# Optimization experiments

Hardware: AMD Instinct MI355X
Metric: run time of the kernel (lower is better)

Reference implementation:

```python
import jax, jax.numpy as jnp
import numpy as np

M, N, B, S = 512, 1024, 64, 50   # measurements, signal dim, batch, sparsity
TAU, ETA = 1.0, 0.1


def setup_inputs() -> dict:
    key = jax.random.key(0)
    k1, k2, k3 = jax.random.split(key, 3)
    X = jax.random.normal(k1, (N, B), dtype=jnp.float32)
    Y = jax.random.normal(k2, (B, M), dtype=jnp.float32)
    A = jax.random.normal(k3, (M, N), dtype=jnp.float32) / np.sqrt(M).astype(np.float32)
    W = jnp.ones((N,), dtype=jnp.float32)
    return {"X": X, "Y": Y, "A": A, "W": W}


def reference(X, Y, A, W):
    # Gradient step: H1 = (I - eta A^T A) X + eta A^T Y^T, computed without
    # materializing the N x N operator.  H1: (N, B)
    H1 = X - ETA * (A.T @ (A @ X)) + ETA * (A.T @ Y.T)
    # NeuralSort soft top-s mask per sample, batched over B.
    z = jnp.abs(W[:, None] * H1).T                      # (B, N) scores
    c = jnp.sum(jnp.abs(z[:, :, None] - z[:, None, :]), axis=-1)  # (B, N)
    ks = (N + 1 - 2 * jnp.arange(1, S + 1)).astype(z.dtype)       # (S,)
    logits = (ks[None, :, None] * z[:, None, :] - c[:, None, :]) / TAU  # (B, S, N)
    mask = jnp.sum(jax.nn.softmax(logits, axis=-1), axis=1)            # (B, N)
    return mask.T * H1                                  # (N, B)
```

## Files before the change

kernel.cpp:

```cpp
#include <hip/hip_runtime.h>
#include <math.h>

#define MM 512
#define NN 1024
#define BB 64
#define SS 50
#define ETA 0.1f

__global__ __launch_bounds__(512) void k_r(const float* __restrict__ X,
                                           const float* __restrict__ Y,
                                           const float* __restrict__ A,
                                           float* __restrict__ R) {
  const int l = threadIdx.x;
  const int w = threadIdx.y;
  const int m0 = blockIdx.x * 2;
  __shared__ float part[8][2][BB];
  const float* __restrict__ Xp = X + w * 128 * BB + l;
  const float* __restrict__ A0 = A + (size_t)m0 * NN + w * 128;
  const float* __restrict__ A1 = A0 + NN;
  float r0a = 0.f, r0b = 0.f, r1a = 0.f, r1b = 0.f;
  #pragma unroll 8
  for (int i = 0; i < 128; i += 4) {
    const float x0 = Xp[(i + 0) * BB];
    const float x1 = Xp[(i + 1) * BB];
    const float x2 = Xp[(i + 2) * BB];
    const float x3 = Xp[(i + 3) * BB];
    const float4 a0 = *reinterpret_cast<const float4*>(A0 + i);
    const float4 a1 = *reinterpret_cast<const float4*>(A1 + i);
    r0a = fmaf(a0.x, x0, fmaf(a0.y, x1, r0a));
    r0b = fmaf(a0.z, x2, fmaf(a0.w, x3, r0b));
    r1a = fmaf(a1.x, x0, fmaf(a1.y, x1, r1a));
    r1b = fmaf(a1.z, x2, fmaf(a1.w, x3, r1b));
  }
  part[w][0][l] = r0a + r0b;
  part[w][1][l] = r1a + r1b;
  __syncthreads();
  if (w < 2) {
    const float s =
        ((part[0][w][l] + part[1][w][l]) + (part[2][w][l] + part[3][w][l])) +
        ((part[4][w][l] + part[5][w][l]) + (part[6][w][l] + part[7][w][l]));
    R[(m0 + w) * BB + l] = Y[l * MM + (m0 + w)] - s;
  }
}

__global__ __launch_bounds__(512) void k_h1z(const float* __restrict__ X,
                                             const float* __restrict__ A,
                                             const float* __restrict__ R,
                                             const float* __restrict__ W,
                                             float* __restrict__ H1_t,
                                             float* __restrict__ z_t) {
  const int l = threadIdx.x;
  const int w = threadIdx.y;
  const int b_l = w >> 2;
  const int mc = w & 3;
  const int nc = blockIdx.x & 7;
  const int bp = blockIdx.x >> 3;
  const int b = bp * 2 + b_l;
  const int n0 = nc * 128;
  __shared__ float part[2][4][128];
  const float* __restrict__ Ap = A + (size_t)(mc * 128) * NN + n0 + l * 2;
  const float* __restrict__ Rp = R + (size_t)(mc * 128) * BB + b;
  float s0 = 0.f, s1 = 0.f, s2 = 0.f, s3 = 0.f;
  float t0 = 0.f, t1 = 0.f, t2 = 0.f, t3 = 0.f;
  #pragma unroll 2
  for (int i = 0; i < 128; i += 4) {
    const float2 a0 = *reinterpret_cast<const float2*>(Ap + (size_t)(i + 0) * NN);
    const float2 a1 = *reinterpret_cast<const float2*>(Ap + (size_t)(i + 1) * NN);
    const float2 a2 = *reinterpret_cast<const float2*>(Ap + (size_t)(i + 2) * NN);
    const float2 a3 = *reinterpret_cast<const float2*>(Ap + (size_t)(i + 3) * NN);
    const float r0 = Rp[(i + 0) * BB];
    const float r1 = Rp[(i + 1) * BB];
    const float r2 = Rp[(i + 2) * BB];
    const float r3 = Rp[(i + 3) * BB];
    s0 = fmaf(a0.x, r0, s0); t0 = fmaf(a0.y, r0, t0);
    s1 = fmaf(a1.x, r1, s1); t1 = fmaf(a1.y, r1, t1);
    s2 = fmaf(a2.x, r2, s2); t2 = fmaf(a2.y, r2, t2);
    s3 = fmaf(a3.x, r3, s3); t3 = fmaf(a3.y, r3, t3);
  }
  part[b_l][mc][l * 2 + 0] = (s0 + s1) + (s2 + s3);
  part[b_l][mc][l * 2 + 1] = (t0 + t1) + (t2 + t3);
  __syncthreads();
  const int tid = w * 64 + l;
  if (tid < 256) {
    const int bl2 = tid >> 7;
    const int nn = tid & 127;
    const int bb = bp * 2 + bl2;
    const int n = n0 + nn;
    const float s = (part[bl2][0][nn] + part[bl2][1][nn]) +
                    (part[bl2][2][nn] + part[bl2][3][nn]);
    const float h = fmaf(ETA, s, X[n * BB + bb]);
    H1_t[bb * NN + n] = h;
    z_t[bb * NN + n] = fabsf(W[n] * h);
  }
}

__global__ __launch_bounds__(256) void k_c(const float* __restrict__ z_t,
                                           float* __restrict__ c_part) {
  const int b = blockIdx.x >> 3;
  const int q = blockIdx.x & 7;
  const int t = threadIdx.x;
  __shared__ __align__(16) float4 z4[NN / 4];
  z4[t] = reinterpret_cast<const float4*>(z_t + b * NN)[t];
  __syncthreads();
  const float* zs = reinterpret_cast<const float*>(z4);
  const float zn0 = zs[t];
  const float zn1 = zs[t + 256];
  const float zn2 = zs[t + 512];
  const float zn3 = zs[t + 768];
  float c0 = 0.f, c1 = 0.f, c2 = 0.f, c3 = 0.f;
  const float4* zq = z4 + q * 32;
  #pragma unroll 4
  for (int i = 0; i < 32; ++i) {
    const float4 f = zq[i];
    c0 += (fabsf(zn0 - f.x) + fabsf(zn0 - f.y)) + (fabsf(zn0 - f.z) + fabsf(zn0 - f.w));
    c1 += (fabsf(zn1 - f.x) + fabsf(zn1 - f.y)) + (fabsf(zn1 - f.z) + fabsf(zn1 - f.w));
    c2 += (fabsf(zn2 - f.x) + fabsf(zn2 - f.y)) + (fabsf(zn2 - f.z) + fabsf(zn2 - f.w));
    c3 += (fabsf(zn3 - f.x) + fabsf(zn3 - f.y)) + (fabsf(zn3 - f.z) + fabsf(zn3 - f.w));
  }
  float* cp = c_part + q * (BB * NN) + b * NN;
  cp[t] = c0;
  cp[t + 256] = c1;
  cp[t + 512] = c2;
  cp[t + 768] = c3;
}

__global__ __launch_bounds__(1024) void k_sm(const float* __restrict__ z_t,
                                             const float* __restrict__ c_part,
                                             const float* __restrict__ H1_t,
                                             float* __restrict__ out) {
  const int b = blockIdx.x;
  const int t = threadIdx.x;
  __shared__ __align__(16) float2 zc_s[NN];
  __shared__ float mpart[16][NN];

  const float z = z_t[b * NN + t];
  const int ci = b * NN + t;
  const int BN = BB * NN;
  const float c = ((c_part[ci] + c_part[ci + BN]) +
                   (c_part[ci + 2 * BN] + c_part[ci + 3 * BN])) +
                  ((c_part[ci + 4 * BN] + c_part[ci + 5 * BN]) +
                   (c_part[ci + 6 * BN] + c_part[ci + 7 * BN]));
  zc_s[t] = make_float2(z, c);
  const float h = H1_t[b * NN + t];
  __syncthreads();

  const int w = t >> 6;
  const int lane = t & 63;
  float zz[16], cc[16], mp[16];
  #pragma unroll
  for (int k = 0; k < 16; ++k) {
    const float2 v = zc_s[lane + 64 * k];
    zz[k] = v.x;
    cc[k] = v.y;
    mp[k] = 0.f;
  }

  for (int s = w; s < SS; s += 16) {
    const float ks = (float)(NN + 1 - 2 * (s + 1));
    float lg[16];
    float mx = -INFINITY;
    #pragma unroll
    for (int k = 0; k < 16; ++k) {
      lg[k] = fmaf(ks, zz[k], -cc[k]);
      mx = fmaxf(mx, lg[k]);
    }
    #pragma unroll
    for (int off = 32; off > 0; off >>= 1)
      mx = fmaxf(mx, __shfl_xor(mx, off, 64));
    float sum = 0.f;
    #pragma unroll
    for (int k = 0; k < 16; ++k) {
      lg[k] = __expf(lg[k] - mx);
      sum += lg[k];
    }
    #pragma unroll
    for (int off = 32; off > 0; off >>= 1)
      sum += __shfl_xor(sum, off, 64);
    const float rs = 1.f / sum;
    #pragma unroll
    for (int k = 0; k < 16; ++k) mp[k] = fmaf(lg[k], rs, mp[k]);
  }
  #pragma unroll
  for (int k = 0; k < 16; ++k) mpart[w][lane + 64 * k] = mp[k];
  __syncthreads();

  float mask = 0.f;
  #pragma unroll
  for (int u = 0; u < 16; ++u) mask += mpart[u][t];
  out[t * BB + b] = mask * h;
}

extern "C" void kernel_launch(void* const* d_in, const int* in_sizes, int n_in,
                              void* d_out, int out_size, void* d_ws, size_t ws_size,
                              hipStream_t stream) {
  const float* X = (const float*)d_in[0];
  const float* Y = (const float*)d_in[1];
  const float* A = (const float*)d_in[2];
  const float* W = (const float*)d_in[3];
  float* out = (float*)d_out;

  float* R = (float*)d_ws;
  float* z_t = R + MM * BB;
  float* H1_t = z_t + NN * BB;
  float* c_part = H1_t + NN * BB;

  k_r   <<<dim3(MM / 2), dim3(64, 8), 0, stream>>>(X, Y, A, R);
  k_h1z <<<dim3(256), dim3(64, 8), 0, stream>>>(X, A, R, W, H1_t, z_t);
  k_c   <<<dim3(BB * 8), dim3(256), 0, stream>>>(z_t, c_part);
  k_sm  <<<dim3(BB), dim3(1024), 0, stream>>>(z_t, c_part, H1_t, out);
}
```

Measured before the change: 37.13 us.

## Fuse four stage kernels into one cooperative kernel with grid syncs

Replaces the four separate launches (residual, H1/z, pairwise c, softmax mask) with a single cooperative kernel of 256 blocks of 512 threads, separated by grid.sync barriers. The goal is to remove launch gaps and inter-kernel drain between the dependent stages. In exchange, stage 3 and stage 4 are remapped to fewer, narrower blocks (4 partial c sums instead of 8, 8 waves per sample instead of 16), which lowers parallelism in those stages. Grid-wide barriers also add their own cost.

```diff
diff --git a/kernel.cpp b/kernel.cpp
--- a/kernel.cpp
+++ b/kernel.cpp
@@ -1,5 +1,8 @@
 #include <hip/hip_runtime.h>
+#include <hip/hip_cooperative_groups.h>
 #include <math.h>
+
+namespace cg = cooperative_groups;
 
 #define MM 512
 #define NN 1024
@@ -7,187 +10,185 @@
 #define SS 50
 #define ETA 0.1f
 
-__global__ __launch_bounds__(512) void k_r(const float* __restrict__ X,
-                                           const float* __restrict__ Y,
-                                           const float* __restrict__ A,
-                                           float* __restrict__ R) {
-  const int l = threadIdx.x;
-  const int w = threadIdx.y;
-  const int m0 = blockIdx.x * 2;
-  __shared__ float part[8][2][BB];
-  const float* __restrict__ Xp = X + w * 128 * BB + l;
-  const float* __restrict__ A0 = A + (size_t)m0 * NN + w * 128;
-  const float* __restrict__ A1 = A0 + NN;
-  float r0a = 0.f, r0b = 0.f, r1a = 0.f, r1b = 0.f;
-  #pragma unroll 8
-  for (int i = 0; i < 128; i += 4) {
-    const float x0 = Xp[(i + 0) * BB];
-    const float x1 = Xp[(i + 1) * BB];
-    const float x2 = Xp[(i + 2) * BB];
-    const float x3 = Xp[(i + 3) * BB];
-    const float4 a0 = *reinterpret_cast<const float4*>(A0 + i);
-    const float4 a1 = *reinterpret_cast<const float4*>(A1 + i);
-    r0a = fmaf(a0.x, x0, fmaf(a0.y, x1, r0a));
-    r0b = fmaf(a0.z, x2, fmaf(a0.w, x3, r0b));
-    r1a = fmaf(a1.x, x0, fmaf(a1.y, x1, r1a));
-    r1b = fmaf(a1.z, x2, fmaf(a1.w, x3, r1b));
-  }
-  part[w][0][l] = r0a + r0b;
-  part[w][1][l] = r1a + r1b;
-  __syncthreads();
-  if (w < 2) {
-    const float s =
-        ((part[0][w][l] + part[1][w][l]) + (part[2][w][l] + part[3][w][l])) +
-        ((part[4][w][l] + part[5][w][l]) + (part[6][w][l] + part[7][w][l]));
-    R[(m0 + w) * BB + l] = Y[l * MM + (m0 + w)] - s;
-  }
-}
-
-__global__ __launch_bounds__(512) void k_h1z(const float* __restrict__ X,
-                                             const float* __restrict__ A,
-                                             const float* __restrict__ R,
-                                             const float* __restrict__ W,
-                                             float* __restrict__ H1_t,
-                                             float* __restrict__ z_t) {
-  const int l = threadIdx.x;
-  const int w = threadIdx.y;
-  const int b_l = w >> 2;
-  const int mc = w & 3;
-  const int nc = blockIdx.x & 7;
-  const int bp = blockIdx.x >> 3;
-  const int b = bp * 2 + b_l;
-  const int n0 = nc * 128;
-  __shared__ float part[2][4][128];
-  const float* __restrict__ Ap = A + (size_t)(mc * 128) * NN + n0 + l * 2;
-  const float* __restrict__ Rp = R + (size_t)(mc * 128) * BB + b;
-  float s0 = 0.f, s1 = 0.f, s2 = 0.f, s3 = 0.f;
-  float t0 = 0.f, t1 = 0.f, t2 = 0.f, t3 = 0.f;
-  #pragma unroll 2
-  for (int i = 0; i < 128; i += 4) {
-    const float2 a0 = *reinterpret_cast<const float2*>(Ap + (size_t)(i + 0) * NN);
-    const float2 a1 = *reinterpret_cast<const float2*>(Ap + (size_t)(i + 1) * NN);
-    const float2 a2 = *reinterpret_cast<const float2*>(Ap + (size_t)(i + 2) * NN);
-    const float2 a3 = *reinterpret_cast<const float2*>(Ap + (size_t)(i + 3) * NN);
-    const float r0 = Rp[(i + 0) * BB];
-    const float r1 = Rp[(i + 1) * BB];
-    const float r2 = Rp[(i + 2) * BB];
-    const float r3 = Rp[(i + 3) * BB];
-    s0 = fmaf(a0.x, r0, s0); t0 = fmaf(a0.y, r0, t0);
-    s1 = fmaf(a1.x, r1, s1); t1 = fmaf(a1.y, r1, t1);
-    s2 = fmaf(a2.x, r2, s2); t2 = fmaf(a2.y, r2, t2);
-    s3 = fmaf(a3.x, r3, s3); t3 = fmaf(a3.y, r3, t3);
-  }
-  part[b_l][mc][l * 2 + 0] = (s0 + s1) + (s2 + s3);
-  part[b_l][mc][l * 2 + 1] = (t0 + t1) + (t2 + t3);
-  __syncthreads();
-  const int tid = w * 64 + l;
-  if (tid < 256) {
-    const int bl2 = tid >> 7;
-    const int nn = tid & 127;
-    const int bb = bp * 2 + bl2;
-    const int n = n0 + nn;
-    const float s = (part[bl2][0][nn] + part[bl2][1][nn]) +
-                    (part[bl2][2][nn] + part[bl2][3][nn]);
-    const float h = fmaf(ETA, s, X[n * BB + bb]);
-    H1_t[bb * NN + n] = h;
-    z_t[bb * NN + n] = fabsf(W[n] * h);
-  }
-}
-
-__global__ __launch_bounds__(256) void k_c(const float* __restrict__ z_t,
-                                           float* __restrict__ c_part) {
-  const int b = blockIdx.x >> 3;
-  const int q = blockIdx.x & 7;
+__global__ __launch_bounds__(512, 2) void k_fused(
+    const float* __restrict__ X,
+    const float* __restrict__ Y,
+    const float* __restrict__ A,
+    const float* __restrict__ W,
+    float* __restrict__ R,
+    float* __restrict__ z_t,
+    float* __restrict__ H1_t,
+    float* __restrict__ c_part,
+    float* __restrict__ out) {
+  cg::grid_group grid = cg::this_grid();
+  const int bid = blockIdx.x;
   const int t = threadIdx.x;
+  const int l = t & 63;
+  const int w = t >> 6;
+
+  __shared__ float p1[8][2][BB];
+  __shared__ float p2[2][4][128];
   __shared__ __align__(16) float4 z4[NN / 4];
-  z4[t] = reinterpret_cast<const float4*>(z_t + b * NN)[t];
-  __syncthreads();
-  const float* zs = reinterpret_cast<const float*>(z4);
-  const float zn0 = zs[t];
-  const float zn1 = zs[t + 256];
-  const float zn2 = zs[t + 512];
-  const float zn3 = zs[t + 768];
-  float c0 = 0.f, c1 = 0.f, c2 = 0.f, c3 = 0.f;
-  const float4* zq = z4 + q * 32;
-  #pragma unroll 4
-  for (int i = 0; i < 32; ++i) {
-    const float4 f = zq[i];
-    c0 += (fabsf(zn0 - f.x) + fabsf(zn0 - f.y)) + (fabsf(zn0 - f.z) + fabsf(zn0 - f.w));
-    c1 += (fabsf(zn1 - f.x) + fabsf(zn1 - f.y)) + (fabsf(zn1 - f.z) + fabsf(zn1 - f.w));
-    c2 += (fabsf(zn2 - f.x) + fabsf(zn2 - f.y)) + (fabsf(zn2 - f.z) + fabsf(zn2 - f.w));
-    c3 += (fabsf(zn3 - f.x) + fabsf(zn3 - f.y)) + (fabsf(zn3 - f.z) + fabsf(zn3 - f.w));
-  }
-  float* cp = c_part + q * (BB * NN) + b * NN;
-  cp[t] = c0;
-  cp[t + 256] = c1;
-  cp[t + 512] = c2;
-  cp[t + 768] = c3;
-}
-
-__global__ __launch_bounds__(1024) void k_sm(const float* __restrict__ z_t,
-                                             const float* __restrict__ c_part,
-                                             const float* __restrict__ H1_t,
-                                             float* __restrict__ out) {
-  const int b = blockIdx.x;
-  const int t = threadIdx.x;
   __shared__ __align__(16) float2 zc_s[NN];
-  __shared__ float mpart[16][NN];
-
-  const float z = z_t[b * NN + t];
-  const int ci = b * NN + t;
-  const int BN = BB * NN;
-  const float c = ((c_part[ci] + c_part[ci + BN]) +
-                   (c_part[ci + 2 * BN] + c_part[ci + 3 * BN])) +
-                  ((c_part[ci + 4 * BN] + c_part[ci + 5 * BN]) +
-                   (c_part[ci + 6 * BN] + c_part[ci + 7 * BN]));
-  zc_s[t] = make_float2(z, c);
-  const float h = H1_t[b * NN + t];
-  __syncthreads();
-
-  const int w = t >> 6;
-  const int lane = t & 63;
-  float zz[16], cc[16], mp[16];
-  #pragma unroll
-  for (int k = 0; k < 16; ++k) {
-    const float2 v = zc_s[lane + 64 * k];
-    zz[k] = v.x;
-    cc[k] = v.y;
-    mp[k] = 0.f;
-  }
-
-  for (int s = w; s < SS; s += 16) {
-    const float ks = (float)(NN + 1 - 2 * (s + 1));
-    float lg[16];
-    float mx = -INFINITY;
+  __shared__ float mpart[8][NN];
+
+  {
+    const int m0 = bid * 2;
+    const float* __restrict__ Xp = X + w * 128 * BB + l;
+    const float* __restrict__ A0 = A + (size_t)m0 * NN + w * 128;
+    const float* __restrict__ A1 = A0 + NN;
+    float r0a = 0.f, r0b = 0.f, r1a = 0.f, r1b = 0.f;
+    #pragma unroll 8
+    for (int i = 0; i < 128; i += 4) {
+      const float x0 = Xp[(i + 0) * BB];
+      const float x1 = Xp[(i + 1) * BB];
+      const float x2 = Xp[(i + 2) * BB];
+      const float x3 = Xp[(i + 3) * BB];
+      const float4 a0 = *reinterpret_cast<const float4*>(A0 + i);
+      const float4 a1 = *reinterpret_cast<const float4*>(A1 + i);
+      r0a = fmaf(a0.x, x0, fmaf(a0.y, x1, r0a));
+      r0b = fmaf(a0.z, x2, fmaf(a0.w, x3, r0b));
+      r1a = fmaf(a1.x, x0, fmaf(a1.y, x1, r1a));
+      r1b = fmaf(a1.z, x2, fmaf(a1.w, x3, r1b));
+    }
+    p1[w][0][l] = r0a + r0b;
+    p1[w][1][l] = r1a + r1b;
+    __syncthreads();
+    if (w < 2) {
+      const float s =
+          ((p1[0][w][l] + p1[1][w][l]) + (p1[2][w][l] + p1[3][w][l])) +
+          ((p1[4][w][l] + p1[5][w][l]) + (p1[6][w][l] + p1[7][w][l]));
+      R[(m0 + w) * BB + l] = Y[l * MM + (m0 + w)] - s;
+    }
+  }
+  grid.sync();
+
+  {
+    const int b_l = w >> 2;
+    const int mc = w & 3;
+    const int nc = bid & 7;
+    const int bp = bid >> 3;
+    const int b = bp * 2 + b_l;
+    const int n0 = nc * 128;
+    const float* __restrict__ Ap = A + (size_t)(mc * 128) * NN + n0 + l * 2;
+    const float* __restrict__ Rp = R + (size_t)(mc * 128) * BB + b;
+    float s0 = 0.f, s1 = 0.f, s2 = 0.f, s3 = 0.f;
+    float t0 = 0.f, t1 = 0.f, t2 = 0.f, t3 = 0.f;
+    #pragma unroll 2
+    for (int i = 0; i < 128; i += 4) {
+      const float2 a0 = *reinterpret_cast<const float2*>(Ap + (size_t)(i + 0) * NN);
+      const float2 a1 = *reinterpret_cast<const float2*>(Ap + (size_t)(i + 1) * NN);
+      const float2 a2 = *reinterpret_cast<const float2*>(Ap + (size_t)(i + 2) * NN);
+      const float2 a3 = *reinterpret_cast<const float2*>(Ap + (size_t)(i + 3) * NN);
+      const float r0 = Rp[(i + 0) * BB];
+      const float r1 = Rp[(i + 1) * BB];
+      const float r2 = Rp[(i + 2) * BB];
+      const float r3 = Rp[(i + 3) * BB];
+      s0 = fmaf(a0.x, r0, s0); t0 = fmaf(a0.y, r0, t0);
+      s1 = fmaf(a1.x, r1, s1); t1 = fmaf(a1.y, r1, t1);
+      s2 = fmaf(a2.x, r2, s2); t2 = fmaf(a2.y, r2, t2);
+      s3 = fmaf(a3.x, r3, s3); t3 = fmaf(a3.y, r3, t3);
+    }
+    p2[b_l][mc][l * 2 + 0] = (s0 + s1) + (s2 + s3);
+    p2[b_l][mc][l * 2 + 1] = (t0 + t1) + (t2 + t3);
+    __syncthreads();
+    if (t < 256) {
+      const int bl2 = t >> 7;
+      const int nn = t & 127;
+      const int bb = bp * 2 + bl2;
+      const int n = n0 + nn;
+      const float s = (p2[bl2][0][nn] + p2[bl2][1][nn]) +
+                      (p2[bl2][2][nn] + p2[bl2][3][nn]);
+      const float h = fmaf(ETA, s, X[n * BB + bb]);
+      H1_t[bb * NN + n] = h;
+      z_t[bb * NN + n] = fabsf(W[n] * h);
+    }
+  }
+  grid.sync();
+
+  {
+    const int b = bid >> 2;
+    const int q = bid & 3;
+    if (t < 256) z4[t] = reinterpret_cast<const float4*>(z_t + b * NN)[t];
+    __syncthreads();
+    const float* zs = reinterpret_cast<const float*>(z4);
+    const float zn0 = zs[t];
+    const float zn1 = zs[t + 512];
+    float c0 = 0.f, c1 = 0.f;
+    const float4* zq = z4 + q * 64;
+    #pragma unroll 4
+    for (int i = 0; i < 64; ++i) {
+      const float4 f = zq[i];
+      c0 += (fabsf(zn0 - f.x) + fabsf(zn0 - f.y)) + (fabsf(zn0 - f.z) + fabsf(zn0 - f.w));
+      c1 += (fabsf(zn1 - f.x) + fabsf(zn1 - f.y)) + (fabsf(zn1 - f.z) + fabsf(zn1 - f.w));
+    }
+    float* cp = c_part + q * (BB * NN) + b * NN;
+    cp[t] = c0;
+    cp[t + 512] = c1;
+  }
+  grid.sync();
+
+  if (bid < BB) {
+    const int b = bid;
+    const int BN = BB * NN;
+    {
+      const int i0 = b * NN + t;
+      const int i1 = i0 + 512;
+      const float cA = (c_part[i0] + c_part[i0 + BN]) +
+                       (c_part[i0 + 2 * BN] + c_part[i0 + 3 * BN]);
+      const float cB = (c_part[i1] + c_part[i1 + BN]) +
+                       (c_part[i1 + 2 * BN] + c_part[i1 + 3 * BN]);
+      zc_s[t] = make_float2(z_t[i0], cA);
+      zc_s[t + 512] = make_float2(z_t[i1], cB);
+    }
+    __syncthreads();
+
+    float zz[16], cc[16], mp[16];
     #pragma unroll
     for (int k = 0; k < 16; ++k) {
-      lg[k] = fmaf(ks, zz[k], -cc[k]);
-      mx = fmaxf(mx, lg[k]);
+      const float2 v = zc_s[l + 64 * k];
+      zz[k] = v.x;
+      cc[k] = v.y;
+      mp[k] = 0.f;
+    }
+    for (int s = w; s < SS; s += 8) {
+      const float ks = (float)(NN + 1 - 2 * (s + 1));
+      float lg[16];
+      float mx = -INFINITY;
+      #pragma unroll
+      for (int k = 0; k < 16; ++k) {
+        lg[k] = fmaf(ks, zz[k], -cc[k]);
+        mx = fmaxf(mx, lg[k]);
+      }
+      #pragma unroll
+      for (int off = 32; off > 0; off >>= 1)
+        mx = fmaxf(mx, __shfl_xor(mx, off, 64));
+      float sum = 0.f;
+      #pragma unroll
+      for (int k = 0; k < 16; ++k) {
+        lg[k] = __expf(lg[k] - mx);
+        sum += lg[k];
+      }
+      #pragma unroll
+      for (int off = 32; off > 0; off >>= 1)
+        sum += __shfl_xor(sum, off, 64);
+      const float rs = 1.f / sum;
+      #pragma unroll
+      for (int k = 0; k < 16; ++k) mp[k] = fmaf(lg[k], rs, mp[k]);
     }
     #pragma unroll
-    for (int off = 32; off > 0; off >>= 1)
-      mx = fmaxf(mx, __shfl_xor(mx, off, 64));
-    float sum = 0.f;
+    for (int k = 0; k < 16; ++k) mpart[w][l + 64 * k] = mp[k];
+    __syncthreads();
+
+    float m0 = 0.f, m1 = 0.f;
     #pragma unroll
-    for (int k = 0; k < 16; ++k) {
-      lg[k] = __expf(lg[k] - mx);
-      sum += lg[k];
-    }
-    #pragma unroll
-    for (int off = 32; off > 0; off >>= 1)
-      sum += __shfl_xor(sum, off, 64);
-    const float rs = 1.f / sum;
-    #pragma unroll
-    for (int k = 0; k < 16; ++k) mp[k] = fmaf(lg[k], rs, mp[k]);
-  }
-  #pragma unroll
-  for (int k = 0; k < 16; ++k) mpart[w][lane + 64 * k] = mp[k];
-  __syncthreads();
-
-  float mask = 0.f;
-  #pragma unroll
-  for (int u = 0; u < 16; ++u) mask += mpart[u][t];
-  out[t * BB + b] = mask * h;
+    for (int u = 0; u < 8; ++u) {
+      m0 += mpart[u][t];
+      m1 += mpart[u][t + 512];
+    }
+    out[t * BB + b] = m0 * H1_t[b * NN + t];
+    out[(t + 512) * BB + b] = m1 * H1_t[b * NN + t + 512];
+  }
 }
 
 extern "C" void kernel_launch(void* const* d_in, const int* in_sizes, int n_in,
@@ -204,8 +205,9 @@
   float* H1_t = z_t + NN * BB;
   float* c_part = H1_t + NN * BB;
 
-  k_r   <<<dim3(MM / 2), dim3(64, 8), 0, stream>>>(X, Y, A, R);
-  k_h1z <<<dim3(256), dim3(64, 8), 0, stream>>>(X, A, R, W, H1_t, z_t);
-  k_c   <<<dim3(BB * 8), dim3(256), 0, stream>>>(z_t, c_part);
-  k_sm  <<<dim3(BB), dim3(1024), 0, stream>>>(z_t, c_part, H1_t, out);
+  void* args[] = {(void*)&X, (void*)&Y, (void*)&A, (void*)&W,
+                  (void*)&R, (void*)&z_t, (void*)&H1_t, (void*)&c_part,
+                  (void*)&out};
+  hipLaunchCooperativeKernel((void*)k_fused, dim3(256), dim3(512), args, 0,
+                             stream);
 }
```

Measured after the change: 131.2 us. 3.53x slower.

## Transpose residual layout, stage it in LDS, and halve pairwise-distance split

Applied to the files above, without the earlier changes.

k_r now writes the residual transposed (batch-major) with float2 stores and float2 loads of Y. k_h1z stages two residual rows in shared memory and reads them as float4, replacing strided scalar global loads with broadcast LDS reads. k_c splits each sample into 4 chunks instead of 8, so each block does more work, k_sm sums 4 partials instead of 8, and the c_part layout becomes contiguous per sample. The trade-off is fewer blocks in k_c (256) and an extra sync in k_h1z.

```diff
diff --git a/kernel.cpp b/kernel.cpp
--- a/kernel.cpp
+++ b/kernel.cpp
@@ -10,7 +10,7 @@
 __global__ __launch_bounds__(512) void k_r(const float* __restrict__ X,
                                            const float* __restrict__ Y,
                                            const float* __restrict__ A,
-                                           float* __restrict__ R) {
+                                           float* __restrict__ R_t) {
   const int l = threadIdx.x;
   const int w = threadIdx.y;
   const int m0 = blockIdx.x * 2;
@@ -35,59 +35,72 @@
   part[w][0][l] = r0a + r0b;
   part[w][1][l] = r1a + r1b;
   __syncthreads();
-  if (w < 2) {
-    const float s =
-        ((part[0][w][l] + part[1][w][l]) + (part[2][w][l] + part[3][w][l])) +
-        ((part[4][w][l] + part[5][w][l]) + (part[6][w][l] + part[7][w][l]));
-    R[(m0 + w) * BB + l] = Y[l * MM + (m0 + w)] - s;
+  if (w == 0) {
+    const float s0 =
+        ((part[0][0][l] + part[1][0][l]) + (part[2][0][l] + part[3][0][l])) +
+        ((part[4][0][l] + part[5][0][l]) + (part[6][0][l] + part[7][0][l]));
+    const float s1 =
+        ((part[0][1][l] + part[1][1][l]) + (part[2][1][l] + part[3][1][l])) +
+        ((part[4][1][l] + part[5][1][l]) + (part[6][1][l] + part[7][1][l]));
+    const float2 y2 = *reinterpret_cast<const float2*>(Y + l * MM + m0);
+    *reinterpret_cast<float2*>(R_t + l * MM + m0) =
+        make_float2(y2.x - s0, y2.y - s1);
   }
 }
 
 __global__ __launch_bounds__(512) void k_h1z(const float* __restrict__ X,
                                              const float* __restrict__ A,
-                                             const float* __restrict__ R,
+                                             const float* __restrict__ R_t,
                                              const float* __restrict__ W,
                                              float* __restrict__ H1_t,
                                              float* __restrict__ z_t) {
   const int l = threadIdx.x;
   const int w = threadIdx.y;
+  const int nc = blockIdx.x & 7;
+  const int bp = blockIdx.x >> 3;
+  const int t5 = w * 64 + l;
+  __shared__ __align__(16) float Rs[2][MM];
+  __shared__ float p2[2][4][128];
+
+  if (t5 < 256) {
+    const int row = t5 >> 7;
+    const int idx = t5 & 127;
+    reinterpret_cast<float4*>(Rs[row])[idx] =
+        reinterpret_cast<const float4*>(R_t + (size_t)(bp * 2 + row) * MM)[idx];
+  }
+  __syncthreads();
+
   const int b_l = w >> 2;
   const int mc = w & 3;
-  const int nc = blockIdx.x & 7;
-  const int bp = blockIdx.x >> 3;
-  const int b = bp * 2 + b_l;
   const int n0 = nc * 128;
-  __shared__ float part[2][4][128];
-  const float* __restrict__ Ap = A + (size_t)(mc * 128) * NN + n0 + l * 2;
-  const float* __restrict__ Rp = R + (size_t)(mc * 128) * BB + b;
+  const float2* __restrict__ A2 =
+      reinterpret_cast<const float2*>(A) + (size_t)(mc * 128) * (NN / 2) + n0 / 2 + l;
+  const float4* __restrict__ R4 =
+      reinterpret_cast<const float4*>(Rs[b_l]) + mc * 32;
   float s0 = 0.f, s1 = 0.f, s2 = 0.f, s3 = 0.f;
-  float t0 = 0.f, t1 = 0.f, t2 = 0.f, t3 = 0.f;
+  float u0 = 0.f, u1 = 0.f, u2 = 0.f, u3 = 0.f;
   #pragma unroll 2
   for (int i = 0; i < 128; i += 4) {
-    const float2 a0 = *reinterpret_cast<const float2*>(Ap + (size_t)(i + 0) * NN);
-    const float2 a1 = *reinterpret_cast<const float2*>(Ap + (size_t)(i + 1) * NN);
-    const float2 a2 = *reinterpret_cast<const float2*>(Ap + (size_t)(i + 2) * NN);
-    const float2 a3 = *reinterpret_cast<const float2*>(Ap + (size_t)(i + 3) * NN);
-    const float r0 = Rp[(i + 0) * BB];
-    const float r1 = Rp[(i + 1) * BB];
-    const float r2 = Rp[(i + 2) * BB];
-    const float r3 = Rp[(i + 3) * BB];
-    s0 = fmaf(a0.x, r0, s0); t0 = fmaf(a0.y, r0, t0);
-    s1 = fmaf(a1.x, r1, s1); t1 = fmaf(a1.y, r1, t1);
-    s2 = fmaf(a2.x, r2, s2); t2 = fmaf(a2.y, r2, t2);
-    s3 = fmaf(a3.x, r3, s3); t3 = fmaf(a3.y, r3, t3);
-  }
-  part[b_l][mc][l * 2 + 0] = (s0 + s1) + (s2 + s3);
-  part[b_l][mc][l * 2 + 1] = (t0 + t1) + (t2 + t3);
-  __syncthreads();
-  const int tid = w * 64 + l;
-  if (tid < 256) {
-    const int bl2 = tid >> 7;
-    const int nn = tid & 127;
+    const float4 r = R4[i >> 2];
+    const float2 q0 = A2[(size_t)(i + 0) * (NN / 2)];
+    const float2 q1 = A2[(size_t)(i + 1) * (NN / 2)];
+    const float2 q2 = A2[(size_t)(i + 2) * (NN / 2)];
+    const float2 q3 = A2[(size_t)(i + 3) * (NN / 2)];
+    s0 = fmaf(q0.x, r.x, s0); u0 = fmaf(q0.y, r.x, u0);
+    s1 = fmaf(q1.x, r.y, s1); u1 = fmaf(q1.y, r.y, u1);
+    s2 = fmaf(q2.x, r.z, s2); u2 = fmaf(q2.y, r.z, u2);
+    s3 = fmaf(q3.x, r.w, s3); u3 = fmaf(q3.y, r.w, u3);
+  }
+  p2[b_l][mc][l * 2 + 0] = (s0 + s1) + (s2 + s3);
+  p2[b_l][mc][l * 2 + 1] = (u0 + u1) + (u2 + u3);
+  __syncthreads();
+  if (t5 < 256) {
+    const int bl2 = t5 >> 7;
+    const int nn = t5 & 127;
     const int bb = bp * 2 + bl2;
     const int n = n0 + nn;
-    const float s = (part[bl2][0][nn] + part[bl2][1][nn]) +
-                    (part[bl2][2][nn] + part[bl2][3][nn]);
+    const float s = (p2[bl2][0][nn] + p2[bl2][1][nn]) +
+                    (p2[bl2][2][nn] + p2[bl2][3][nn]);
     const float h = fmaf(ETA, s, X[n * BB + bb]);
     H1_t[bb * NN + n] = h;
     z_t[bb * NN + n] = fabsf(W[n] * h);
@@ -96,8 +109,8 @@
 
 __global__ __launch_bounds__(256) void k_c(const float* __restrict__ z_t,
                                            float* __restrict__ c_part) {
-  const int b = blockIdx.x >> 3;
-  const int q = blockIdx.x & 7;
+  const int b = blockIdx.x >> 2;
+  const int q = blockIdx.x & 3;
   const int t = threadIdx.x;
   __shared__ __align__(16) float4 z4[NN / 4];
   z4[t] = reinterpret_cast<const float4*>(z_t + b * NN)[t];
@@ -108,16 +121,16 @@
   const float zn2 = zs[t + 512];
   const float zn3 = zs[t + 768];
   float c0 = 0.f, c1 = 0.f, c2 = 0.f, c3 = 0.f;
-  const float4* zq = z4 + q * 32;
+  const float4* zq = z4 + q * 64;
   #pragma unroll 4
-  for (int i = 0; i < 32; ++i) {
+  for (int i = 0; i < 64; ++i) {
     const float4 f = zq[i];
     c0 += (fabsf(zn0 - f.x) + fabsf(zn0 - f.y)) + (fabsf(zn0 - f.z) + fabsf(zn0 - f.w));
     c1 += (fabsf(zn1 - f.x) + fabsf(zn1 - f.y)) + (fabsf(zn1 - f.z) + fabsf(zn1 - f.w));
     c2 += (fabsf(zn2 - f.x) + fabsf(zn2 - f.y)) + (fabsf(zn2 - f.z) + fabsf(zn2 - f.w));
     c3 += (fabsf(zn3 - f.x) + fabsf(zn3 - f.y)) + (fabsf(zn3 - f.z) + fabsf(zn3 - f.w));
   }
-  float* cp = c_part + q * (BB * NN) + b * NN;
+  float* cp = c_part + (size_t)(b * 4 + q) * NN;
   cp[t] = c0;
   cp[t + 256] = c1;
   cp[t + 512] = c2;
@@ -133,14 +146,9 @@
   __shared__ __align__(16) float2 zc_s[NN];
   __shared__ float mpart[16][NN];
 
-  const float z = z_t[b * NN + t];
-  const int ci = b * NN + t;
-  const int BN = BB * NN;
-  const float c = ((c_part[ci] + c_part[ci + BN]) +
-                   (c_part[ci + 2 * BN] + c_part[ci + 3 * BN])) +
-                  ((c_part[ci + 4 * BN] + c_part[ci + 5 * BN]) +
-                   (c_part[ci + 6 * BN] + c_part[ci + 7 * BN]));
-  zc_s[t] = make_float2(z, c);
+  const float* __restrict__ cb = c_part + (size_t)b * 4 * NN;
+  const float c = (cb[t] + cb[t + NN]) + (cb[t + 2 * NN] + cb[t + 3 * NN]);
+  zc_s[t] = make_float2(z_t[b * NN + t], c);
   const float h = H1_t[b * NN + t];
   __syncthreads();
 
@@ -199,13 +207,13 @@
   const float* W = (const float*)d_in[3];
   float* out = (float*)d_out;
 
-  float* R = (float*)d_ws;
-  float* z_t = R + MM * BB;
-  float* H1_t = z_t + NN * BB;
-  float* c_part = H1_t + NN * BB;
-
-  k_r   <<<dim3(MM / 2), dim3(64, 8), 0, stream>>>(X, Y, A, R);
-  k_h1z <<<dim3(256), dim3(64, 8), 0, stream>>>(X, A, R, W, H1_t, z_t);
-  k_c   <<<dim3(BB * 8), dim3(256), 0, stream>>>(z_t, c_part);
+  float* R_t = (float*)d_ws;
+  float* z_t = R_t + BB * MM;
+  float* H1_t = z_t + BB * NN;
+  float* c_part = H1_t + BB * NN;
+
+  k_r   <<<dim3(MM / 2), dim3(64, 8), 0, stream>>>(X, Y, A, R_t);
+  k_h1z <<<dim3(256), dim3(64, 8), 0, stream>>>(X, A, R_t, W, H1_t, z_t);
+  k_c   <<<dim3(BB * 4), dim3(256), 0, stream>>>(z_t, c_part);
   k_sm  <<<dim3(BB), dim3(1024), 0, stream>>>(z_t, c_part, H1_t, out);
 }
```

Result: faster. 35.69 us (-3.9%).
